# Performance work log

Measured on AMD Instinct MI355X. Metric: run time of the kernel, lower is better.

Reference implementation:

```python
import jax, jax.numpy as jnp
import numpy as np

H = 1024
S = 32768

def setup_inputs() -> dict:
    key = jax.random.key(0)
    k1, k2, k3, k4 = jax.random.split(key, 4)
    return {
        "hidden_state": jax.random.normal(k1, (1, 1, H), dtype=jnp.float32),
        "encoder_output": jax.random.normal(k2, (1, S, H), dtype=jnp.float32),
        "W": jax.random.normal(k3, (H, H), dtype=jnp.float32) / np.sqrt(H),
        "b": jax.random.normal(k4, (H,), dtype=jnp.float32) * 0.01,
    }

def reference(hidden_state, encoder_output, W, b):
    # method == 'general': energy_i = h . (W @ e_i + b)
    h = hidden_state[0, 0]            # [H]
    enc = encoder_output[0]           # [S, H]
    proj = enc @ W.T + b              # [S, H]  (nn.Linear)
    energies = proj @ h               # [S]
    return jax.nn.softmax(energies[None, :], axis=1)  # [1, S]
```

## Files before the change

kernel.cpp:

```cpp
#include <hip/hip_runtime.h>


#define H 1024
#define S 32768

__global__ __launch_bounds__(256) void matvec_v(const float* __restrict__ W,
                                                const float* __restrict__ h,
                                                float* __restrict__ v) {
    const int t  = threadIdx.x;
    const int j0 = blockIdx.x * 16;
    float a0 = 0.f, a1 = 0.f, a2 = 0.f, a3 = 0.f;
#pragma unroll
    for (int jj = 0; jj < 16; ++jj) {
        const int j = j0 + jj;
        const float hj = h[j];
        const float* Wr = W + (size_t)j * H;
        a0 = fmaf(Wr[t      ], hj, a0);
        a1 = fmaf(Wr[t + 256], hj, a1);
        a2 = fmaf(Wr[t + 512], hj, a2);
        a3 = fmaf(Wr[t + 768], hj, a3);
    }
    atomicAdd(&v[t      ], a0);
    atomicAdd(&v[t + 256], a1);
    atomicAdd(&v[t + 512], a2);
    atomicAdd(&v[t + 768], a3);
}

__global__ __launch_bounds__(256) void energies_kernel(const float* __restrict__ enc,
                                                       const float* __restrict__ v,
                                                       float* __restrict__ e) {
    const int wave  = threadIdx.x >> 6;
    const int lane  = threadIdx.x & 63;
    const int lane4 = lane * 4;

    float4 vf[4];
#pragma unroll
    for (int t = 0; t < 4; ++t)
        vf[t] = *(const float4*)(v + t * 256 + lane4);

    const int row0 = (blockIdx.x * 4 + wave) * 2;
#pragma unroll
    for (int r = 0; r < 2; ++r) {
        const int row = row0 + r;
        const float* rp = enc + (size_t)row * H;
        float acc = 0.f;
#pragma unroll
        for (int t = 0; t < 4; ++t) {
            const float4 a = *(const float4*)(rp + t * 256 + lane4);
            acc = fmaf(a.x, vf[t].x, acc);
            acc = fmaf(a.y, vf[t].y, acc);
            acc = fmaf(a.z, vf[t].z, acc);
            acc = fmaf(a.w, vf[t].w, acc);
        }
#pragma unroll
        for (int off = 32; off >= 1; off >>= 1)
            acc += __shfl_down(acc, off, 64);
        if (lane == 0) e[row] = acc;
    }
}

__global__ __launch_bounds__(1024) void softmax_kernel(const float* __restrict__ e,
                                                       float* __restrict__ out) {
    __shared__ float red[16];
    const int t    = threadIdx.x;
    const int lane = t & 63;
    const int wv   = t >> 6;

    float4 x[8];
#pragma unroll
    for (int r = 0; r < 8; ++r)
        x[r] = *(const float4*)(e + 4 * t + 4096 * r);

    float m = -1e30f;
#pragma unroll
    for (int r = 0; r < 8; ++r)
        m = fmaxf(m, fmaxf(fmaxf(x[r].x, x[r].y), fmaxf(x[r].z, x[r].w)));
#pragma unroll
    for (int off = 32; off >= 1; off >>= 1)
        m = fmaxf(m, __shfl_down(m, off, 64));
    if (lane == 0) red[wv] = m;
    __syncthreads();
    if (t < 16) {
        float mm = red[t];
#pragma unroll
        for (int off = 8; off >= 1; off >>= 1)
            mm = fmaxf(mm, __shfl_down(mm, off, 64));
        if (t == 0) red[0] = mm;
    }
    __syncthreads();
    m = red[0];
    __syncthreads();

    float s = 0.f;
#pragma unroll
    for (int r = 0; r < 8; ++r) {
        x[r].x = __expf(x[r].x - m); s += x[r].x;
        x[r].y = __expf(x[r].y - m); s += x[r].y;
        x[r].z = __expf(x[r].z - m); s += x[r].z;
        x[r].w = __expf(x[r].w - m); s += x[r].w;
    }
#pragma unroll
    for (int off = 32; off >= 1; off >>= 1)
        s += __shfl_down(s, off, 64);
    if (lane == 0) red[wv] = s;
    __syncthreads();
    if (t < 16) {
        float ss = red[t];
#pragma unroll
        for (int off = 8; off >= 1; off >>= 1)
            ss += __shfl_down(ss, off, 64);
        if (t == 0) red[0] = ss;
    }
    __syncthreads();
    const float inv = 1.0f / red[0];

#pragma unroll
    for (int r = 0; r < 8; ++r) {
        float4 y;
        y.x = x[r].x * inv;
        y.y = x[r].y * inv;
        y.z = x[r].z * inv;
        y.w = x[r].w * inv;
        *(float4*)(out + 4 * t + 4096 * r) = y;
    }
}

extern "C" void kernel_launch(void* const* d_in, const int* in_sizes, int n_in,
                              void* d_out, int out_size, void* d_ws, size_t ws_size,
                              hipStream_t stream) {
    const float* h   = (const float*)d_in[0];
    const float* enc = (const float*)d_in[1];
    const float* W   = (const float*)d_in[2];

    float* v = (float*)d_ws;
    float* e = (float*)d_ws + H;
    float* out = (float*)d_out;

    hipMemsetAsync(v, 0, H * sizeof(float), stream);

    matvec_v<<<64, 256, 0, stream>>>(W, h, v);
    energies_kernel<<<S / 8, 256, 0, stream>>>(enc, v, e);
    softmax_kernel<<<1, 1024, 0, stream>>>(e, out);
}
```

Measured before the change: 204.5 us.

## Drop memset and atomics in matvec, batch four rows per wave in energies

After: 203.4 us. No clear change (-0.6%).

```diff
diff --git a/kernel.cpp b/kernel.cpp
--- a/kernel.cpp
+++ b/kernel.cpp
@@ -7,23 +7,27 @@
 __global__ __launch_bounds__(256) void matvec_v(const float* __restrict__ W,
                                                 const float* __restrict__ h,
                                                 float* __restrict__ v) {
-    const int t  = threadIdx.x;
-    const int j0 = blockIdx.x * 16;
-    float a0 = 0.f, a1 = 0.f, a2 = 0.f, a3 = 0.f;
+    __shared__ float sh[64];
+    const int t    = threadIdx.x;
+    const int kk   = t & 15;
+    const int jj   = t >> 4;
+    const int w    = t >> 6;
+    const int lane = t & 63;
+    const int k0   = blockIdx.x * 16;
+
+    const float* Wp = W + (size_t)jj * H + k0 + kk;
+    float a0 = 0.f, a1 = 0.f;
 #pragma unroll
-    for (int jj = 0; jj < 16; ++jj) {
-        const int j = j0 + jj;
-        const float hj = h[j];
-        const float* Wr = W + (size_t)j * H;
-        a0 = fmaf(Wr[t      ], hj, a0);
-        a1 = fmaf(Wr[t + 256], hj, a1);
-        a2 = fmaf(Wr[t + 512], hj, a2);
-        a3 = fmaf(Wr[t + 768], hj, a3);
+    for (int i = 0; i < 64; i += 2) {
+        a0 = fmaf(Wp[(size_t)(16 * i) * H],       h[16 * i + jj],       a0);
+        a1 = fmaf(Wp[(size_t)(16 * (i + 1)) * H], h[16 * (i + 1) + jj], a1);
     }
-    atomicAdd(&v[t      ], a0);
-    atomicAdd(&v[t + 256], a1);
-    atomicAdd(&v[t + 512], a2);
-    atomicAdd(&v[t + 768], a3);
+    float a = a0 + a1;
+    a += __shfl_xor(a, 16, 64);
+    a += __shfl_xor(a, 32, 64);
+    if (lane < 16) sh[w * 16 + lane] = a;
+    __syncthreads();
+    if (t < 16) v[k0 + t] = sh[t] + sh[t + 16] + sh[t + 32] + sh[t + 48];
 }
 
 __global__ __launch_bounds__(256) void energies_kernel(const float* __restrict__ enc,
@@ -38,25 +42,34 @@
     for (int t = 0; t < 4; ++t)
         vf[t] = *(const float4*)(v + t * 256 + lane4);
 
-    const int row0 = (blockIdx.x * 4 + wave) * 2;
+    const int row0 = (blockIdx.x * 4 + wave) * 4;
+    const float* rp = enc + (size_t)row0 * H + lane4;
+
+    float4 a[4][4];
 #pragma unroll
-    for (int r = 0; r < 2; ++r) {
-        const int row = row0 + r;
-        const float* rp = enc + (size_t)row * H;
-        float acc = 0.f;
+    for (int r = 0; r < 4; ++r)
+#pragma unroll
+        for (int t = 0; t < 4; ++t)
+            a[r][t] = *(const float4*)(rp + (size_t)r * H + t * 256);
+
+    float acc[4];
+#pragma unroll
+    for (int r = 0; r < 4; ++r) {
+        float s = 0.f;
 #pragma unroll
         for (int t = 0; t < 4; ++t) {
-            const float4 a = *(const float4*)(rp + t * 256 + lane4);
-            acc = fmaf(a.x, vf[t].x, acc);
-            acc = fmaf(a.y, vf[t].y, acc);
-            acc = fmaf(a.z, vf[t].z, acc);
-            acc = fmaf(a.w, vf[t].w, acc);
+            s = fmaf(a[r][t].x, vf[t].x, s);
+            s = fmaf(a[r][t].y, vf[t].y, s);
+            s = fmaf(a[r][t].z, vf[t].z, s);
+            s = fmaf(a[r][t].w, vf[t].w, s);
         }
 #pragma unroll
         for (int off = 32; off >= 1; off >>= 1)
-            acc += __shfl_down(acc, off, 64);
-        if (lane == 0) e[row] = acc;
+            s += __shfl_xor(s, off, 64);
+        acc[r] = s;
     }
+    if (lane == 0)
+        *(float4*)(e + row0) = make_float4(acc[0], acc[1], acc[2], acc[3]);
 }
 
 __global__ __launch_bounds__(1024) void softmax_kernel(const float* __restrict__ e,
@@ -77,14 +90,14 @@
         m = fmaxf(m, fmaxf(fmaxf(x[r].x, x[r].y), fmaxf(x[r].z, x[r].w)));
 #pragma unroll
     for (int off = 32; off >= 1; off >>= 1)
-        m = fmaxf(m, __shfl_down(m, off, 64));
+        m = fmaxf(m, __shfl_xor(m, off, 64));
     if (lane == 0) red[wv] = m;
     __syncthreads();
     if (t < 16) {
         float mm = red[t];
 #pragma unroll
         for (int off = 8; off >= 1; off >>= 1)
-            mm = fmaxf(mm, __shfl_down(mm, off, 64));
+            mm = fmaxf(mm, __shfl_xor(mm, off, 64));
         if (t == 0) red[0] = mm;
     }
     __syncthreads();
@@ -101,14 +114,14 @@
     }
 #pragma unroll
     for (int off = 32; off >= 1; off >>= 1)
-        s += __shfl_down(s, off, 64);
+        s += __shfl_xor(s, off, 64);
     if (lane == 0) red[wv] = s;
     __syncthreads();
     if (t < 16) {
         float ss = red[t];
 #pragma unroll
         for (int off = 8; off >= 1; off >>= 1)
-            ss += __shfl_down(ss, off, 64);
+            ss += __shfl_xor(ss, off, 64);
         if (t == 0) red[0] = ss;
     }
     __syncthreads();
@@ -136,9 +149,7 @@
     float* e = (float*)d_ws + H;
     float* out = (float*)d_out;
 
-    hipMemsetAsync(v, 0, H * sizeof(float), stream);
-
     matvec_v<<<64, 256, 0, stream>>>(W, h, v);
-    energies_kernel<<<S / 8, 256, 0, stream>>>(enc, v, e);
+    energies_kernel<<<S / 16, 256, 0, stream>>>(enc, v, e);
     softmax_kernel<<<1, 1024, 0, stream>>>(e, out);
 }
```
